# Performance work log

Hardware: AMD Instinct MI355X
Metric: run time of the kernel (lower is better)

## Reference

```python
import jax, jax.numpy as jnp
import numpy as np

B, T, D, H = 4, 2048, 1024, 16
HD = D // H

def setup_inputs() -> dict:
    key = jax.random.key(0)
    ks = jax.random.split(key, 5)
    s = 0.02
    return {
        "x": jax.random.normal(ks[0], (B, T, D), dtype=jnp.float32),
        "w_qkv": jax.random.normal(ks[1], (D, 3 * D), dtype=jnp.float32) * s,
        "b_qkv": jax.random.normal(ks[2], (3 * D,), dtype=jnp.float32) * s,
        "w_proj": jax.random.normal(ks[3], (D, D), dtype=jnp.float32) * s,
        "b_proj": jax.random.normal(ks[4], (D,), dtype=jnp.float32) * s,
    }

def reference(x, w_qkv, b_qkv, w_proj, b_proj):
    b, t, c = x.shape
    h, hd = H, HD
    scale = hd ** -0.5
    qkv = x @ w_qkv + b_qkv                       # [B,T,3D]
    qkv = qkv.reshape(b, t, 3, h, hd)
    q, k, v = qkv[:, :, 0], qkv[:, :, 1], qkv[:, :, 2]   # [B,T,H,HD]
    # scores [B,H,T,T]
    att = jnp.einsum('bqhd,bkhd->bhqk', q, k) * scale
    causal = jnp.tril(jnp.ones((t, t), dtype=bool))
    att = jnp.where(causal[None, None], att, -jnp.inf)
    w = jax.nn.softmax(att, axis=-1)
    out = jnp.einsum('bhqk,bkhd->bqhd', w, v).reshape(b, t, c)
    return out @ w_proj + b_proj
```

## Files before the change

### kernel.cpp

```cpp
#include <hip/hip_runtime.h>
#include <hip/hip_bf16.h>
#include <cstdint>

#define BB 4
#define TT 2048
#define DD 1024
#define HH 16
#define HD 64
#define MM (BB*TT)
#define NQKV (3*DD)
#define SCALE 0.125f
#define NQT 16

typedef __bf16 bf16;
typedef __bf16 bf16x8 __attribute__((ext_vector_type(8)));
typedef float f32x4 __attribute__((ext_vector_type(4)));

#define AS1 __attribute__((address_space(1)))
#define AS3 __attribute__((address_space(3)))

__device__ __forceinline__ void gload_lds16(const void* g, void* l) {
  __builtin_amdgcn_global_load_lds((const AS1 uint32_t*)g, (AS3 uint32_t*)l, 16, 0, 0);
}

__global__ void k_cvt_x(const float* __restrict__ in, bf16* __restrict__ out) {
  int i = blockIdx.x * blockDim.x + threadIdx.x;
  float4 v = ((const float4*)in)[i];
  ushort4 o;
  o.x = __builtin_bit_cast(unsigned short, (bf16)v.x);
  o.y = __builtin_bit_cast(unsigned short, (bf16)v.y);
  o.z = __builtin_bit_cast(unsigned short, (bf16)v.z);
  o.w = __builtin_bit_cast(unsigned short, (bf16)v.w);
  ((ushort4*)out)[i] = o;
}

__global__ void k_transpose_w(const float* __restrict__ in, bf16* __restrict__ out,
                              int R, int C) {
  __shared__ float tile[32][33];
  const int c0 = blockIdx.x * 32, r0 = blockIdx.y * 32;
  const int tx = threadIdx.x & 31, ty = threadIdx.x >> 5;
#pragma unroll
  for (int i = 0; i < 32; i += 8)
    tile[ty + i][tx] = in[(long)(r0 + ty + i) * C + c0 + tx];
  __syncthreads();
#pragma unroll
  for (int i = 0; i < 32; i += 8)
    out[(long)(c0 + ty + i) * R + r0 + tx] = (bf16)tile[tx][ty + i];
}

__global__ void k_transpose_v(const bf16* __restrict__ V, bf16* __restrict__ Vt) {
  __shared__ bf16 tile[64][65];
  const int bh = blockIdx.z;
  const int t0 = blockIdx.x * 64;
  const bf16* src = V + (long)bh * TT * HD;
  bf16* dst = Vt + (long)bh * HD * TT;
  const int tx = threadIdx.x & 63, ty = threadIdx.x >> 6;
#pragma unroll
  for (int i = 0; i < 64; i += 4)
    tile[ty + i][tx] = src[(long)(t0 + ty + i) * HD + tx];
  __syncthreads();
#pragma unroll
  for (int i = 0; i < 64; i += 4)
    dst[(long)(ty + i) * TT + t0 + tx] = tile[tx][ty + i];
}

template <int EPI>
__global__ __launch_bounds__(256) void k_gemm(
    const bf16* __restrict__ A, const bf16* __restrict__ Bt,
    const float* __restrict__ bias, float* __restrict__ fout,
    bf16* __restrict__ q_out, bf16* __restrict__ k_out, bf16* __restrict__ v_out,
    int K) {
  __shared__ bf16 As[128 * 64];
  __shared__ bf16 Bs[128 * 64];
  const int tid = threadIdx.x;
  const int m0 = blockIdx.x * 128;
  const int n0 = blockIdx.y * 128;
  const int wv = tid >> 6, lane = tid & 63;
  const int g = lane >> 4, lr = lane & 15;
  const int wm = (wv >> 1) * 64, wn = (wv & 1) * 64;
  const int sr = tid >> 3, sc = tid & 7;
  f32x4 acc[4][4] = {};

  for (int k0 = 0; k0 < K; k0 += 64) {
#pragma unroll
    for (int p = 0; p < 4; ++p) {
      const int row = p * 32 + sr;
      const int chunk = sc ^ (row & 7);
      gload_lds16(A + ((long)(m0 + row) * K + k0 + (chunk << 3)),
                  &As[(row << 6) + (sc << 3)]);
      gload_lds16(Bt + ((long)(n0 + row) * K + k0 + (chunk << 3)),
                  &Bs[(row << 6) + (sc << 3)]);
    }
    __syncthreads();
#pragma unroll
    for (int kf = 0; kf < 2; ++kf) {
      bf16x8 af[4], bfr[4];
#pragma unroll
      for (int mf = 0; mf < 4; ++mf) {
        const int row = wm + mf * 16 + lr;
        af[mf] = *(const bf16x8*)((const char*)As +
                 (((row << 7) + (kf << 6) + (g << 4)) ^ ((row & 7) << 4)));
      }
#pragma unroll
      for (int nf = 0; nf < 4; ++nf) {
        const int row = wn + nf * 16 + lr;
        bfr[nf] = *(const bf16x8*)((const char*)Bs +
                 (((row << 7) + (kf << 6) + (g << 4)) ^ ((row & 7) << 4)));
      }
#pragma unroll
      for (int mf = 0; mf < 4; ++mf)
#pragma unroll
        for (int nf = 0; nf < 4; ++nf)
          acc[mf][nf] = __builtin_amdgcn_mfma_f32_16x16x32_bf16(af[mf], bfr[nf],
                                                                acc[mf][nf], 0, 0, 0);
    }
    __syncthreads();
  }

#pragma unroll
  for (int nf = 0; nf < 4; ++nf) {
    const int col = n0 + wn + nf * 16 + lr;
    const float bv = bias[col];
#pragma unroll
    for (int mf = 0; mf < 4; ++mf) {
#pragma unroll
      for (int j = 0; j < 4; ++j) {
        const int rowm = m0 + wm + mf * 16 + g * 4 + j;
        const float v = acc[mf][nf][j] + bv;
        if (EPI == 0) {
          const int sel = col >> 10, d1 = col & 1023;
          const int h = d1 >> 6, hd = d1 & 63;
          const int b = rowm >> 11, t = rowm & 2047;
          const long off = ((((long)b * HH + h) * TT + t) << 6) + hd;
          bf16* dst = (sel == 0) ? q_out : (sel == 1 ? k_out : v_out);
          dst[off] = (bf16)v;
        } else {
          fout[(long)rowm * DD + col] = v;
        }
      }
    }
  }
}

__device__ __forceinline__ void attn_tile(
    const bf16* __restrict__ Kt, const bf16* __restrict__ Vt,
    bf16* __restrict__ Pw, const bf16x8 (&qf)[2][2],
    f32x4 (&acc)[2][4], f32x4 (&ls)[2],
    int rowbase, int kv0, int g, int lr, bf16x8 ones) {
  f32x4 s[2][4] = {};
#pragma unroll
  for (int kf = 0; kf < 2; ++kf) {
    bf16x8 bfr[4];
#pragma unroll
    for (int nf = 0; nf < 4; ++nf) {
      const int row = nf * 16 + lr;
      bfr[nf] = *(const bf16x8*)((const char*)Kt +
               (((row << 7) + (kf << 6) + (g << 4)) ^ ((row & 7) << 4)));
    }
#pragma unroll
    for (int mf = 0; mf < 2; ++mf)
#pragma unroll
      for (int nf = 0; nf < 4; ++nf)
        s[mf][nf] = __builtin_amdgcn_mfma_f32_16x16x32_bf16(qf[mf][kf], bfr[nf],
                                                            s[mf][nf], 0, 0, 0);
  }
#pragma unroll
  for (int mf = 0; mf < 2; ++mf) {
#pragma unroll
    for (int nf = 0; nf < 4; ++nf) {
      const int col = kv0 + nf * 16 + lr;
#pragma unroll
      for (int j = 0; j < 4; ++j) {
        const int rowq = rowbase + mf * 16 + g * 4 + j;
        const float p = (col <= rowq) ? __expf(s[mf][nf][j] * SCALE) : 0.f;
        const int prow = mf * 16 + g * 4 + j;
        const int pcol = nf * 16 + lr;
        *(bf16*)((char*)Pw +
                 (((prow << 7) + (pcol << 1)) ^ ((prow & 7) << 4))) = (bf16)p;
      }
    }
  }
#pragma unroll
  for (int kf = 0; kf < 2; ++kf) {
    bf16x8 pa[2], vb[4];
#pragma unroll
    for (int mf = 0; mf < 2; ++mf) {
      const int row = mf * 16 + lr;
      pa[mf] = *(const bf16x8*)((const char*)Pw +
               (((row << 7) + (kf << 6) + (g << 4)) ^ ((row & 7) << 4)));
    }
#pragma unroll
    for (int nf = 0; nf < 4; ++nf) {
      const int row = nf * 16 + lr;
      vb[nf] = *(const bf16x8*)((const char*)Vt +
               (((row << 7) + (kf << 6) + (g << 4)) ^ ((row & 7) << 4)));
    }
#pragma unroll
    for (int mf = 0; mf < 2; ++mf)
      ls[mf] = __builtin_amdgcn_mfma_f32_16x16x32_bf16(pa[mf], ones, ls[mf], 0, 0, 0);
#pragma unroll
    for (int mf = 0; mf < 2; ++mf)
#pragma unroll
      for (int nf = 0; nf < 4; ++nf)
        acc[mf][nf] = __builtin_amdgcn_mfma_f32_16x16x32_bf16(pa[mf], vb[nf],
                                                              acc[mf][nf], 0, 0, 0);
  }
}

__global__ __launch_bounds__(256, 2) void k_attn(
    const bf16* __restrict__ Q, const bf16* __restrict__ K,
    const bf16* __restrict__ Vt, bf16* __restrict__ O) {
  __shared__ bf16 Ks[2][64 * 64];
  __shared__ bf16 Vs[2][64 * 64];
  __shared__ bf16 Ps[4][32 * 64];
  const int tid = threadIdx.x;
  const int qa = blockIdx.x, qb = NQT - 1 - qa;
  const int bh = blockIdx.y;
  const int b = bh >> 4, h = bh & 15;
  const int wv = tid >> 6, lane = tid & 63;
  const int g = lane >> 4, lr = lane & 15;
  const int ra = qa * 128 + wv * 32;
  const int rb = qb * 128 + wv * 32;
  const bf16* Qb = Q + (long)bh * TT * HD;
  const bf16* Kb = K + (long)bh * TT * HD;
  const bf16* Vb = Vt + (long)bh * HD * TT;
  bf16* Pw = &Ps[wv][0];

  bf16x8 ones;
#pragma unroll
  for (int i = 0; i < 8; ++i) ones[i] = (bf16)1.0f;

  bf16x8 qfa[2][2], qfb[2][2];
#pragma unroll
  for (int mf = 0; mf < 2; ++mf)
#pragma unroll
    for (int kf = 0; kf < 2; ++kf) {
      qfa[mf][kf] = *(const bf16x8*)(Qb + ((long)(ra + mf * 16 + lr) << 6) +
                                     kf * 32 + g * 8);
      qfb[mf][kf] = *(const bf16x8*)(Qb + ((long)(rb + mf * 16 + lr) << 6) +
                                     kf * 32 + g * 8);
    }

  f32x4 acca[2][4] = {}, accb[2][4] = {};
  f32x4 lsa[2] = {}, lsb[2] = {};

  const int sr = tid >> 3, sc = tid & 7;
  const int nkv = 2 * qb + 2;

  auto STAGE = [&](int buf, int kt) {
    const int kv0 = kt * 64;
#pragma unroll
    for (int p = 0; p < 2; ++p) {
      const int row = p * 32 + sr;
      const int chunk = sc ^ (row & 7);
      gload_lds16(Kb + ((long)(kv0 + row) << 6) + (chunk << 3),
                  &Ks[buf][(row << 6) + (sc << 3)]);
      gload_lds16(Vb + (long)row * TT + kv0 + (chunk << 3),
                  &Vs[buf][(row << 6) + (sc << 3)]);
    }
  };

  STAGE(0, 0);
  __syncthreads();

  int cur = 0;
  for (int kt = 0; kt < nkv; ++kt) {
    const int kv0 = kt * 64;
    if (kt + 1 < nkv) STAGE(cur ^ 1, kt + 1);
    if (kv0 <= ra + 31)
      attn_tile(&Ks[cur][0], &Vs[cur][0], Pw, qfa, acca, lsa, ra, kv0, g, lr, ones);
    if (kv0 <= rb + 31)
      attn_tile(&Ks[cur][0], &Vs[cur][0], Pw, qfb, accb, lsb, rb, kv0, g, lr, ones);
    __syncthreads();
    cur ^= 1;
  }

#pragma unroll
  for (int mf = 0; mf < 2; ++mf) {
    float inva[4], invb[4];
#pragma unroll
    for (int j = 0; j < 4; ++j) {
      inva[j] = 1.0f / lsa[mf][j];
      invb[j] = 1.0f / lsb[mf][j];
    }
#pragma unroll
    for (int nf = 0; nf < 4; ++nf) {
      const int col = h * 64 + nf * 16 + lr;
#pragma unroll
      for (int j = 0; j < 4; ++j) {
        const int ta = ra + mf * 16 + g * 4 + j;
        const int tb = rb + mf * 16 + g * 4 + j;
        O[(((long)b * TT + ta) << 10) + col] = (bf16)(acca[mf][nf][j] * inva[j]);
        O[(((long)b * TT + tb) << 10) + col] = (bf16)(accb[mf][nf][j] * invb[j]);
      }
    }
  }
}

extern "C" void kernel_launch(void* const* d_in, const int* in_sizes, int n_in,
                              void* d_out, int out_size, void* d_ws, size_t ws_size,
                              hipStream_t stream) {
  (void)in_sizes; (void)n_in; (void)out_size; (void)ws_size;
  const float* x      = (const float*)d_in[0];
  const float* w_qkv  = (const float*)d_in[1];
  const float* b_qkv  = (const float*)d_in[2];
  const float* w_proj = (const float*)d_in[3];
  const float* b_proj = (const float*)d_in[4];
  float* out = (float*)d_out;

  bf16* ws = (bf16*)d_ws;
  const long NX = (long)MM * DD;
  bf16* xb     = ws;
  bf16* wqkvT  = xb + NX;
  bf16* wprojT = wqkvT + (long)NQKV * DD;
  bf16* Qb     = wprojT + (long)DD * DD;
  bf16* Kb     = Qb + NX;
  bf16* Vb     = Kb + NX;
  bf16* Vtb    = xb;
  bf16* attout = Vb;

  k_cvt_x<<<(int)(NX / 4 / 256), 256, 0, stream>>>(x, xb);
  k_transpose_w<<<dim3(NQKV / 32, DD / 32), 256, 0, stream>>>(w_qkv, wqkvT, DD, NQKV);
  k_transpose_w<<<dim3(DD / 32, DD / 32), 256, 0, stream>>>(w_proj, wprojT, DD, DD);
  k_gemm<0><<<dim3(MM / 128, NQKV / 128), 256, 0, stream>>>(
      xb, wqkvT, b_qkv, nullptr, Qb, Kb, Vb, DD);
  k_transpose_v<<<dim3(TT / 64, 1, BB * HH), 256, 0, stream>>>(Vb, Vtb);
  k_attn<<<dim3(NQT / 2, BB * HH), 256, 0, stream>>>(Qb, Kb, Vtb, attout);
  k_gemm<1><<<dim3(MM / 128, DD / 128), 256, 0, stream>>>(
      attout, wprojT, b_proj, out, nullptr, nullptr, nullptr, DD);
}
```

Measured before the change: 187.5 us.

## Triple-buffer K/V staging with explicit vmcnt waits and hoisted fragment loads

Replaces the double-buffered K/V LDS pipeline with a three-stage ring, prefetching two tiles ahead. The full __syncthreads is swapped for an explicit s_waitcnt vmcnt plus s_barrier. K and V fragments are loaded from LDS once per tile and reused by both query blocks instead of reloaded inside each tile call. s_setprio raises wave priority around the MFMA bursts. The goal is more overlap of global loads with compute and fewer LDS reads, at the cost of extra LDS and registers that could lower occupancy. The vmcnt counts are hand-tuned and fragile if the number of issued loads changes.

Result: slower. 268.1 us (+43.0%).

```diff
diff --git a/kernel.cpp b/kernel.cpp
--- a/kernel.cpp
+++ b/kernel.cpp
@@ -142,76 +142,11 @@
   }
 }
 
-__device__ __forceinline__ void attn_tile(
-    const bf16* __restrict__ Kt, const bf16* __restrict__ Vt,
-    bf16* __restrict__ Pw, const bf16x8 (&qf)[2][2],
-    f32x4 (&acc)[2][4], f32x4 (&ls)[2],
-    int rowbase, int kv0, int g, int lr, bf16x8 ones) {
-  f32x4 s[2][4] = {};
-#pragma unroll
-  for (int kf = 0; kf < 2; ++kf) {
-    bf16x8 bfr[4];
-#pragma unroll
-    for (int nf = 0; nf < 4; ++nf) {
-      const int row = nf * 16 + lr;
-      bfr[nf] = *(const bf16x8*)((const char*)Kt +
-               (((row << 7) + (kf << 6) + (g << 4)) ^ ((row & 7) << 4)));
-    }
-#pragma unroll
-    for (int mf = 0; mf < 2; ++mf)
-#pragma unroll
-      for (int nf = 0; nf < 4; ++nf)
-        s[mf][nf] = __builtin_amdgcn_mfma_f32_16x16x32_bf16(qf[mf][kf], bfr[nf],
-                                                            s[mf][nf], 0, 0, 0);
-  }
-#pragma unroll
-  for (int mf = 0; mf < 2; ++mf) {
-#pragma unroll
-    for (int nf = 0; nf < 4; ++nf) {
-      const int col = kv0 + nf * 16 + lr;
-#pragma unroll
-      for (int j = 0; j < 4; ++j) {
-        const int rowq = rowbase + mf * 16 + g * 4 + j;
-        const float p = (col <= rowq) ? __expf(s[mf][nf][j] * SCALE) : 0.f;
-        const int prow = mf * 16 + g * 4 + j;
-        const int pcol = nf * 16 + lr;
-        *(bf16*)((char*)Pw +
-                 (((prow << 7) + (pcol << 1)) ^ ((prow & 7) << 4))) = (bf16)p;
-      }
-    }
-  }
-#pragma unroll
-  for (int kf = 0; kf < 2; ++kf) {
-    bf16x8 pa[2], vb[4];
-#pragma unroll
-    for (int mf = 0; mf < 2; ++mf) {
-      const int row = mf * 16 + lr;
-      pa[mf] = *(const bf16x8*)((const char*)Pw +
-               (((row << 7) + (kf << 6) + (g << 4)) ^ ((row & 7) << 4)));
-    }
-#pragma unroll
-    for (int nf = 0; nf < 4; ++nf) {
-      const int row = nf * 16 + lr;
-      vb[nf] = *(const bf16x8*)((const char*)Vt +
-               (((row << 7) + (kf << 6) + (g << 4)) ^ ((row & 7) << 4)));
-    }
-#pragma unroll
-    for (int mf = 0; mf < 2; ++mf)
-      ls[mf] = __builtin_amdgcn_mfma_f32_16x16x32_bf16(pa[mf], ones, ls[mf], 0, 0, 0);
-#pragma unroll
-    for (int mf = 0; mf < 2; ++mf)
-#pragma unroll
-      for (int nf = 0; nf < 4; ++nf)
-        acc[mf][nf] = __builtin_amdgcn_mfma_f32_16x16x32_bf16(pa[mf], vb[nf],
-                                                              acc[mf][nf], 0, 0, 0);
-  }
-}
-
 __global__ __launch_bounds__(256, 2) void k_attn(
     const bf16* __restrict__ Q, const bf16* __restrict__ K,
     const bf16* __restrict__ Vt, bf16* __restrict__ O) {
-  __shared__ bf16 Ks[2][64 * 64];
-  __shared__ bf16 Vs[2][64 * 64];
+  __shared__ bf16 Ks[3][64 * 64];
+  __shared__ bf16 Vs[3][64 * 64];
   __shared__ bf16 Ps[4][32 * 64];
   const int tid = threadIdx.x;
   const int qa = blockIdx.x, qb = NQT - 1 - qa;
@@ -260,19 +195,91 @@
     }
   };
 
+  auto DOQ = [&](const bf16x8 (&qf)[2][2], const bf16x8 (&kfr)[2][4],
+                 const bf16x8 (&vfr)[2][4], f32x4 (&acc)[2][4], f32x4 (&ls)[2],
+                 int rowbase, int kv0) {
+    f32x4 s[2][4] = {};
+    __builtin_amdgcn_s_setprio(1);
+#pragma unroll
+    for (int kf = 0; kf < 2; ++kf)
+#pragma unroll
+      for (int mf = 0; mf < 2; ++mf)
+#pragma unroll
+        for (int nf = 0; nf < 4; ++nf)
+          s[mf][nf] = __builtin_amdgcn_mfma_f32_16x16x32_bf16(qf[mf][kf], kfr[kf][nf],
+                                                              s[mf][nf], 0, 0, 0);
+    __builtin_amdgcn_s_setprio(0);
+#pragma unroll
+    for (int mf = 0; mf < 2; ++mf) {
+#pragma unroll
+      for (int nf = 0; nf < 4; ++nf) {
+        const int col = kv0 + nf * 16 + lr;
+#pragma unroll
+        for (int j = 0; j < 4; ++j) {
+          const int rowq = rowbase + mf * 16 + g * 4 + j;
+          const float p = (col <= rowq) ? __expf(s[mf][nf][j] * SCALE) : 0.f;
+          const int prow = mf * 16 + g * 4 + j;
+          const int pcol = nf * 16 + lr;
+          *(bf16*)((char*)Pw +
+                   (((prow << 7) + (pcol << 1)) ^ ((prow & 7) << 4))) = (bf16)p;
+        }
+      }
+    }
+    bf16x8 pa[2][2];
+#pragma unroll
+    for (int kf = 0; kf < 2; ++kf)
+#pragma unroll
+      for (int mf = 0; mf < 2; ++mf) {
+        const int row = mf * 16 + lr;
+        pa[kf][mf] = *(const bf16x8*)((const char*)Pw +
+                     (((row << 7) + (kf << 6) + (g << 4)) ^ ((row & 7) << 4)));
+      }
+    __builtin_amdgcn_s_setprio(1);
+#pragma unroll
+    for (int kf = 0; kf < 2; ++kf) {
+#pragma unroll
+      for (int mf = 0; mf < 2; ++mf)
+        ls[mf] = __builtin_amdgcn_mfma_f32_16x16x32_bf16(pa[kf][mf], ones, ls[mf],
+                                                         0, 0, 0);
+#pragma unroll
+      for (int mf = 0; mf < 2; ++mf)
+#pragma unroll
+        for (int nf = 0; nf < 4; ++nf)
+          acc[mf][nf] = __builtin_amdgcn_mfma_f32_16x16x32_bf16(pa[kf][mf], vfr[kf][nf],
+                                                                acc[mf][nf], 0, 0, 0);
+    }
+    __builtin_amdgcn_s_setprio(0);
+  };
+
   STAGE(0, 0);
-  __syncthreads();
-
-  int cur = 0;
+  STAGE(1, 1);
+  int bcur = 0, bnxt = 1, bnn = 2;
+
   for (int kt = 0; kt < nkv; ++kt) {
     const int kv0 = kt * 64;
-    if (kt + 1 < nkv) STAGE(cur ^ 1, kt + 1);
-    if (kv0 <= ra + 31)
-      attn_tile(&Ks[cur][0], &Vs[cur][0], Pw, qfa, acca, lsa, ra, kv0, g, lr, ones);
-    if (kv0 <= rb + 31)
-      attn_tile(&Ks[cur][0], &Vs[cur][0], Pw, qfb, accb, lsb, rb, kv0, g, lr, ones);
-    __syncthreads();
-    cur ^= 1;
+    if (kt + 1 < nkv) asm volatile("s_waitcnt vmcnt(4)" ::: "memory");
+    else              asm volatile("s_waitcnt vmcnt(0)" ::: "memory");
+    __builtin_amdgcn_s_barrier();
+    __builtin_amdgcn_sched_barrier(0);
+    if (kt + 2 < nkv) STAGE(bnn, kt + 2);
+
+    const bf16* Kt  = &Ks[bcur][0];
+    const bf16* Vtl = &Vs[bcur][0];
+    bf16x8 kfr[2][4], vfr[2][4];
+#pragma unroll
+    for (int kf = 0; kf < 2; ++kf)
+#pragma unroll
+      for (int nf = 0; nf < 4; ++nf) {
+        const int row = nf * 16 + lr;
+        const int off = (((row << 7) + (kf << 6) + (g << 4)) ^ ((row & 7) << 4));
+        kfr[kf][nf] = *(const bf16x8*)((const char*)Kt + off);
+        vfr[kf][nf] = *(const bf16x8*)((const char*)Vtl + off);
+      }
+
+    if (kv0 <= ra + 31) DOQ(qfa, kfr, vfr, acca, lsa, ra, kv0);
+    if (kv0 <= rb + 31) DOQ(qfb, kfr, vfr, accb, lsb, rb, kv0);
+
+    const int t = bcur; bcur = bnxt; bnxt = bnn; bnn = t;
   }
 
 #pragma unroll
```
